# Kernel tuning notes

Hardware: AMD Instinct MI355X
Metric: run time of the kernel (lower is better)

The kernel has to match this reference:

```python
import jax, jax.numpy as jnp
import numpy as np

K = 1024          # codebook size
D = 64            # embedding dim
CC = 0.25         # commitment cost


def setup_inputs() -> dict:
    key = jax.random.key(0)
    k1, k2 = jax.random.split(key)
    inputs = jax.random.normal(k1, (64, 64, 32, 32), dtype=jnp.float32)  # [B, C=D, H, W]
    # nn.Embedding weight init: uniform(-1/K, 1/K)
    embedding = jax.random.uniform(k2, (K, D), dtype=jnp.float32,
                                   minval=-1.0 / K, maxval=1.0 / K)
    return {"inputs": inputs, "embedding": embedding}


def reference(inputs, embedding):
    # NCHW -> NHWC
    x = jnp.transpose(inputs, (0, 2, 3, 1))            # [B, H, W, D]
    B, H, W, Dd = x.shape
    flat = x.reshape(-1, Dd)                           # [N, D]
    distances = (jnp.sum(flat * flat, axis=1, keepdims=True)
                 - 2.0 * flat @ embedding.T
                 + jnp.sum(embedding * embedding, axis=1)[None, :])
    encoding_indices = jnp.argmin(distances, axis=1)   # [N]
    encodings = encoding_indices.reshape(B, H, W)      # [B, H, W]
    quantized = embedding[encodings]                   # [B, H, W, D]

    e_latent_loss = jnp.mean((jax.lax.stop_gradient(quantized) - x) ** 2)
    q_latent_loss = jnp.mean((quantized - jax.lax.stop_gradient(x)) ** 2)
    loss = q_latent_loss + CC * e_latent_loss

    # straight-through estimator
    quantized_st = x + jax.lax.stop_gradient(quantized - x)
    out = jnp.transpose(quantized_st, (0, 3, 1, 2))    # NHWC -> NCHW
    nll = jnp.ones((1,), dtype=jnp.float32)
    return out, encodings, loss, nll
```

## Files before the change

kernel.cpp:

```cpp
#include <hip/hip_runtime.h>
#include <stdint.h>

constexpr int KCODES = 1024;
constexpr int DDIM   = 64;
constexpr int HW     = 1024;
constexpr int NPTS   = 65536;
constexpr int PPB    = 64;
constexpr int NBLK   = NPTS / PPB;

constexpr int OUT_Q    = 0;
constexpr int OUT_IDX  = 4194304;
constexpr int OUT_LOSS = 4259840;
constexpr int OUT_NLL  = 4259841;

constexpr int WS_MAXC  = 0;
constexpr int WS_C     = 16;
constexpr int WS_E     = 2048;
constexpr int WS_PART  = 34816;

typedef __attribute__((ext_vector_type(8))) short short8v;
typedef __attribute__((ext_vector_type(4))) float float4v;

__device__ __forceinline__ uint16_t f2bf(float f) {
    uint32_t u = __float_as_uint(f);
    return (uint16_t)((u + 0x7fffu + ((u >> 16) & 1u)) >> 16);
}
__device__ __forceinline__ uint32_t pack2bf(float a, float b) {
    return (uint32_t)f2bf(a) | ((uint32_t)f2bf(b) << 16);
}

__device__ __forceinline__ float np_pairwise_sumsq64(const float* a) {
    float r[8];
    #pragma unroll
    for (int j = 0; j < 8; ++j) r[j] = __fmul_rn(a[j], a[j]);
    #pragma unroll
    for (int i = 8; i < 64; i += 8)
        #pragma unroll
        for (int j = 0; j < 8; ++j)
            r[j] = __fadd_rn(r[j], __fmul_rn(a[i + j], a[i + j]));
    return __fadd_rn(__fadd_rn(__fadd_rn(r[0], r[1]), __fadd_rn(r[2], r[3])),
                     __fadd_rn(__fadd_rn(r[4], r[5]), __fadd_rn(r[6], r[7])));
}

__global__ __launch_bounds__(256) void vq_init(const float* __restrict__ emb,
                                               float* __restrict__ ws) {
    __shared__ float smax[4];
    const int k = blockIdx.x * 256 + threadIdx.x;
    float row[DDIM];
    const float4* src = (const float4*)(emb + (size_t)k * DDIM);
    #pragma unroll
    for (int j = 0; j < 16; ++j) ((float4*)row)[j] = src[j];
    float C = np_pairwise_sumsq64(row);
    ws[WS_C + k] = C;
    {
        const int c = k >> 4, col = k & 15;
        uint32_t* eb = (uint32_t*)ws + WS_E + c * 512;
        #pragma unroll
        for (int q = 0; q < 4; ++q) {
            uint32_t* d0 = eb + (q * 16 + col) * 4;
            uint32_t* d1 = eb + 256 + (q * 16 + col) * 4;
            #pragma unroll
            for (int j = 0; j < 4; ++j) {
                d0[j] = pack2bf(row[q * 8 + 2 * j],      row[q * 8 + 2 * j + 1]);
                d1[j] = pack2bf(row[32 + q * 8 + 2 * j], row[32 + q * 8 + 2 * j + 1]);
            }
        }
    }
    float m = C;
    #pragma unroll
    for (int off = 32; off > 0; off >>= 1) m = fmaxf(m, __shfl_down(m, off, 64));
    if ((threadIdx.x & 63) == 0) smax[threadIdx.x >> 6] = m;
    __syncthreads();
    if (threadIdx.x == 0)
        ws[WS_MAXC + blockIdx.x] =
            fmaxf(fmaxf(smax[0], smax[1]), fmaxf(smax[2], smax[3]));
}

__global__ __launch_bounds__(256, 4) void vq_main(
        const float* __restrict__ inp, const float* __restrict__ emb,
        float* __restrict__ ws, float* __restrict__ out)
{
    __shared__ float    sAp[PPB][4];
    __shared__ float    sA[PPB];
    __shared__ float    sPart[4][PPB];
    __shared__ float    sThr[PPB];
    __shared__ uint16_t sCand[PPB * 4 * 8];
    __shared__ uint8_t  sCnt[PPB * 4];
    __shared__ int      sWin[PPB];
    __shared__ float    sred[4];

    const int tid  = threadIdx.x;
    const int lane = tid & 63;
    const int wave = tid >> 6;
    const int col  = lane & 15;
    const int quad = lane >> 4;
    const int base = blockIdx.x * PPB;
    const int b    = base >> 10;
    const int hw0  = base & 1023;

    {
        const int pp = tid >> 2;
        const int jj = (tid & 3) * 2;
        const float* xin = inp + (size_t)b * DDIM * HW + (hw0 + pp);
        float r0, r1;
        {
            float v0 = xin[(size_t)jj * HW];
            float v1 = xin[(size_t)(jj + 1) * HW];
            r0 = __fmul_rn(v0, v0);
            r1 = __fmul_rn(v1, v1);
        }
        #pragma unroll
        for (int i = 8; i < 64; i += 8) {
            float v0 = xin[(size_t)(i + jj) * HW];
            float v1 = xin[(size_t)(i + jj + 1) * HW];
            r0 = __fadd_rn(r0, __fmul_rn(v0, v0));
            r1 = __fadd_rn(r1, __fmul_rn(v1, v1));
        }
        sAp[pp][tid & 3] = __fadd_rn(r0, r1);
    }

    short8v a[4][2];
    #pragma unroll
    for (int g = 0; g < 4; ++g) {
        const float* xp = inp + (size_t)b * DDIM * HW + (hw0 + g * 16 + col);
        short8v t0, t1;
        #pragma unroll
        for (int j = 0; j < 8; ++j) {
            t0[j] = (short)f2bf(xp[(size_t)(quad * 8 + j) * HW]);
            t1[j] = (short)f2bf(xp[(size_t)(32 + quad * 8 + j) * HW]);
        }
        a[g][0] = t0; a[g][1] = t1;
    }

    const char* Eb = (const char*)((const uint32_t*)ws + WS_E);
    const char* Ew = Eb + (size_t)wave * 16 * 2048 + (size_t)lane * 16;
    const float* Cw = ws + WS_C;
    const int k0 = wave * 256;

    float smaxv[4][4];
    #pragma unroll
    for (int g = 0; g < 4; ++g)
        #pragma unroll
        for (int r = 0; r < 4; ++r) smaxv[g][r] = -3.0e38f;

    {
        short8v pa0 = *(const short8v*)(Ew);
        short8v pa1 = *(const short8v*)(Ew + 1024);
        short8v pb0 = *(const short8v*)(Ew + 2048);
        short8v pb1 = *(const short8v*)(Ew + 2048 + 1024);
        float   cia = Cw[k0 + col] * -0.5f;
        float   cib = Cw[k0 + 16 + col] * -0.5f;
        #pragma unroll 1
        for (int c2 = 0; c2 < 16; c2 += 2) {
            short8v u0 = pa0, u1 = pa1; float uci = cia;
            if (c2 + 2 < 16) {
                const char* er = Ew + (size_t)(c2 + 2) * 2048;
                pa0 = *(const short8v*)(er);
                pa1 = *(const short8v*)(er + 1024);
                cia = Cw[k0 + (c2 + 2) * 16 + col] * -0.5f;
            }
            float4v ci4 = {uci, uci, uci, uci};
            #pragma unroll
            for (int g = 0; g < 4; ++g) {
                float4v acc = ci4;
                acc = __builtin_amdgcn_mfma_f32_16x16x32_bf16(a[g][0], u0, acc, 0, 0, 0);
                acc = __builtin_amdgcn_mfma_f32_16x16x32_bf16(a[g][1], u1, acc, 0, 0, 0);
                #pragma unroll
                for (int r = 0; r < 4; ++r) smaxv[g][r] = fmaxf(smaxv[g][r], acc[r]);
            }
            short8v v0 = pb0, v1 = pb1; float vci = cib;
            if (c2 + 3 < 16) {
                const char* er = Ew + (size_t)(c2 + 3) * 2048;
                pb0 = *(const short8v*)(er);
                pb1 = *(const short8v*)(er + 1024);
                cib = Cw[k0 + (c2 + 3) * 16 + col] * -0.5f;
            }
            float4v ci4b = {vci, vci, vci, vci};
            #pragma unroll
            for (int g = 0; g < 4; ++g) {
                float4v acc = ci4b;
                acc = __builtin_amdgcn_mfma_f32_16x16x32_bf16(a[g][0], v0, acc, 0, 0, 0);
                acc = __builtin_amdgcn_mfma_f32_16x16x32_bf16(a[g][1], v1, acc, 0, 0, 0);
                #pragma unroll
                for (int r = 0; r < 4; ++r) smaxv[g][r] = fmaxf(smaxv[g][r], acc[r]);
            }
        }
    }
    #pragma unroll
    for (int g = 0; g < 4; ++g)
        #pragma unroll
        for (int r = 0; r < 4; ++r) {
            float m = smaxv[g][r];
            m = fmaxf(m, __shfl_xor(m, 1, 16));
            m = fmaxf(m, __shfl_xor(m, 2, 16));
            m = fmaxf(m, __shfl_xor(m, 4, 16));
            m = fmaxf(m, __shfl_xor(m, 8, 16));
            if (col == 0) sPart[wave][g * 16 + quad * 4 + r] = m;
        }
    __syncthreads();

    if (tid < PPB) {
        float A = __fadd_rn(__fadd_rn(sAp[tid][0], sAp[tid][1]),
                            __fadd_rn(sAp[tid][2], sAp[tid][3]));
        sA[tid] = A;
        float gm = fmaxf(fmaxf(sPart[0][tid], sPart[1][tid]),
                         fmaxf(sPart[2][tid], sPart[3][tid]));
        float mc = fmaxf(fmaxf(ws[WS_MAXC], ws[WS_MAXC + 1]),
                         fmaxf(ws[WS_MAXC + 2], ws[WS_MAXC + 3]));
        sThr[tid] = gm - (0.015625f * sqrtf(A) * sqrtf(mc) + 6e-5f);
    }
    __syncthreads();

    float thr[4][4];
    #pragma unroll
    for (int g = 0; g < 4; ++g)
        #pragma unroll
        for (int r = 0; r < 4; ++r) thr[g][r] = sThr[g * 16 + quad * 4 + r];

    int cnt[4][4];
    #pragma unroll
    for (int g = 0; g < 4; ++g)
        #pragma unroll
        for (int r = 0; r < 4; ++r) cnt[g][r] = 0;

    {
        short8v pa0 = *(const short8v*)(Ew);
        short8v pa1 = *(const short8v*)(Ew + 1024);
        short8v pb0 = *(const short8v*)(Ew + 2048);
        short8v pb1 = *(const short8v*)(Ew + 2048 + 1024);
        float   cia = Cw[k0 + col] * -0.5f;
        float   cib = Cw[k0 + 16 + col] * -0.5f;
        #pragma unroll 1
        for (int c2 = 0; c2 < 16; c2 += 2) {
            short8v u0 = pa0, u1 = pa1; float uci = cia;
            if (c2 + 2 < 16) {
                const char* er = Ew + (size_t)(c2 + 2) * 2048;
                pa0 = *(const short8v*)(er);
                pa1 = *(const short8v*)(er + 1024);
                cia = Cw[k0 + (c2 + 2) * 16 + col] * -0.5f;
            }
            float4v ci4 = {uci, uci, uci, uci};
            #pragma unroll
            for (int g = 0; g < 4; ++g) {
                float4v acc = ci4;
                acc = __builtin_amdgcn_mfma_f32_16x16x32_bf16(a[g][0], u0, acc, 0, 0, 0);
                acc = __builtin_amdgcn_mfma_f32_16x16x32_bf16(a[g][1], u1, acc, 0, 0, 0);
                #pragma unroll
                for (int r = 0; r < 4; ++r) {
                    unsigned long long bm = __ballot(acc[r] >= thr[g][r]);
                    if (col == 0) {
                        unsigned gm = (unsigned)(bm >> (quad * 16)) & 0xffffu;
                        while (gm) {
                            int bit = __ffs(gm) - 1;
                            gm &= gm - 1;
                            int ct = cnt[g][r];
                            if (ct < 8)
                                sCand[((g * 16 + quad * 4 + r) * 4 + wave) * 8 + ct] =
                                    (uint16_t)(k0 + c2 * 16 + bit);
                            cnt[g][r] = ct + 1;
                        }
                    }
                }
            }
            short8v v0 = pb0, v1 = pb1; float vci = cib;
            if (c2 + 3 < 16) {
                const char* er = Ew + (size_t)(c2 + 3) * 2048;
                pb0 = *(const short8v*)(er);
                pb1 = *(const short8v*)(er + 1024);
                cib = Cw[k0 + (c2 + 3) * 16 + col] * -0.5f;
            }
            float4v ci4b = {vci, vci, vci, vci};
            #pragma unroll
            for (int g = 0; g < 4; ++g) {
                float4v acc = ci4b;
                acc = __builtin_amdgcn_mfma_f32_16x16x32_bf16(a[g][0], v0, acc, 0, 0, 0);
                acc = __builtin_amdgcn_mfma_f32_16x16x32_bf16(a[g][1], v1, acc, 0, 0, 0);
                #pragma unroll
                for (int r = 0; r < 4; ++r) {
                    unsigned long long bm = __ballot(acc[r] >= thr[g][r]);
                    if (col == 0) {
                        unsigned gm = (unsigned)(bm >> (quad * 16)) & 0xffffu;
                        while (gm) {
                            int bit = __ffs(gm) - 1;
                            gm &= gm - 1;
                            int ct = cnt[g][r];
                            if (ct < 8)
                                sCand[((g * 16 + quad * 4 + r) * 4 + wave) * 8 + ct] =
                                    (uint16_t)(k0 + (c2 + 1) * 16 + bit);
                            cnt[g][r] = ct + 1;
                        }
                    }
                }
            }
        }
    }
    if (col == 0) {
        #pragma unroll
        for (int g = 0; g < 4; ++g)
            #pragma unroll
            for (int r = 0; r < 4; ++r) {
                int c = cnt[g][r];
                sCnt[(g * 16 + quad * 4 + r) * 4 + wave] = (uint8_t)(c > 255 ? 255 : c);
            }
    }
    __syncthreads();

    if (tid < PPB) {
        const int p = tid, n = base + p;
        int cq[4], tot = 0, cmax = 0;
        #pragma unroll
        for (int q = 0; q < 4; ++q) {
            cq[q] = sCnt[p * 4 + q];
            tot += cq[q];
            cmax = cq[q] > cmax ? cq[q] : cmax;
        }
        int win;
        if (tot == 1) {
            win = 0;
            #pragma unroll
            for (int q = 0; q < 4; ++q)
                if (cq[q]) win = sCand[(p * 4 + q) * 8];
        } else {
            const float* xin = inp + (size_t)b * DDIM * HW + (hw0 + p);
            float x[DDIM];
            #pragma unroll
            for (int d = 0; d < DDIM; ++d) x[d] = xin[(size_t)d * HW];
            const float A = sA[p];
            float bd = 3.0e38f; win = KCODES - 1;
            if (cmax <= 8) {
                #pragma unroll 1
                for (int q = 0; q < 4; ++q) {
                    #pragma unroll 1
                    for (int i = 0; i < cq[q]; ++i) {
                        int k = sCand[(p * 4 + q) * 8 + i];
                        float e[DDIM];
                        const float4* e4 = (const float4*)(emb + (size_t)k * DDIM);
                        #pragma unroll
                        for (int j = 0; j < 16; ++j) ((float4*)e)[j] = e4[j];
                        float g = 0.f;
                        #pragma unroll
                        for (int d = 0; d < DDIM; ++d) g = fmaf(x[d], e[d], g);
                        float dd = __fadd_rn(__fsub_rn(A, __fmul_rn(2.0f, g)), Cw[k]);
                        if (dd < bd || (dd == bd && k < win)) { bd = dd; win = k; }
                    }
                }
            } else {
                #pragma unroll 1
                for (int k = 0; k < KCODES; ++k) {
                    float e[DDIM];
                    const float4* e4 = (const float4*)(emb + (size_t)k * DDIM);
                    #pragma unroll
                    for (int j = 0; j < 16; ++j) ((float4*)e)[j] = e4[j];
                    float g = 0.f;
                    #pragma unroll
                    for (int d = 0; d < DDIM; ++d) g = fmaf(x[d], e[d], g);
                    float dd = __fadd_rn(__fsub_rn(A, __fmul_rn(2.0f, g)), Cw[k]);
                    if (dd < bd) { bd = dd; win = k; }
                }
            }
        }
        sWin[p] = win;
        out[OUT_IDX + n] = (float)win;
    }
    __syncthreads();

    {
        const int pl = tid & 63, qtr = tid >> 6;
        const int win = sWin[pl];
        const int ch0 = qtr * 16;
        float q[16];
        const float4* q4 = (const float4*)(emb + (size_t)win * DDIM + ch0);
        #pragma unroll
        for (int j = 0; j < 4; ++j) ((float4*)q)[j] = q4[j];
        const size_t off = (size_t)b * DDIM * HW + (size_t)ch0 * HW + (hw0 + pl);
        const float* xin2 = inp + off;
        float* orow = out + off;
        float lacc = 0.f;
        #pragma unroll
        for (int j = 0; j < 16; ++j) {
            float xv = xin2[(size_t)j * HW];
            float diff = __fsub_rn(q[j], xv);
            orow[(size_t)j * HW] = __fadd_rn(xv, diff);
            lacc = fmaf(diff, diff, lacc);
        }
        #pragma unroll
        for (int o2 = 32; o2 > 0; o2 >>= 1) lacc += __shfl_down(lacc, o2, 64);
        if (lane == 0) sred[wave] = lacc;
    }
    __syncthreads();
    if (tid == 0)
        ws[WS_PART + blockIdx.x] = sred[0] + sred[1] + sred[2] + sred[3];
}

__global__ __launch_bounds__(256) void vq_fin(const float* __restrict__ ws,
                                              float* __restrict__ out) {
    __shared__ float sred[4];
    const int tid = threadIdx.x;
    float s = 0.f;
    #pragma unroll
    for (int j = 0; j < 4; ++j) s += ws[WS_PART + j * 256 + tid];
    #pragma unroll
    for (int off = 32; off > 0; off >>= 1) s += __shfl_down(s, off, 64);
    if ((tid & 63) == 0) sred[tid >> 6] = s;
    __syncthreads();
    if (tid == 0) {
        float L = sred[0] + sred[1] + sred[2] + sred[3];
        out[OUT_LOSS] = L * (1.25f / 4194304.0f);
        out[OUT_NLL]  = 1.0f;
    }
}

extern "C" void kernel_launch(void* const* d_in, const int* in_sizes, int n_in,
                              void* d_out, int out_size, void* d_ws, size_t ws_size,
                              hipStream_t stream) {
    const float* inp = (const float*)d_in[0];
    const float* emb = (const float*)d_in[1];
    float* out = (float*)d_out;
    float* ws  = (float*)d_ws;

    vq_init<<<4, 256, 0, stream>>>(emb, ws);
    vq_main<<<NBLK, 256, 0, stream>>>(inp, emb, ws, out);
    vq_fin<<<1, 256, 0, stream>>>(ws, out);
}
```

Measured before the change: 119.8 us.

## Swap MFMA operands, per-lane candidate lists, and fold final loss reduction into main

Swaps the MFMA operand order so each lane's accumulator holds four codes for one point. The row max then becomes a local reduction plus two cross-quad shuffles, replacing the 16-lane shuffle tree. Candidate collection moves from per-row ballots with a serial col==0 loop to per-lane 64-bit packed lists of up to four indices, gated by a wave-wide any check. The separate final-reduction kernel is removed in favour of a last-block-done atomic counter, and the init kernel is reshaped to 16 blocks of 64 threads. The main risk is that the per-lane candidate cap drops from 8 to 4, which sends more points to the full 1024-code fallback scan.

```diff
diff --git a/kernel.cpp b/kernel.cpp
--- a/kernel.cpp
+++ b/kernel.cpp
@@ -17,6 +17,7 @@
 constexpr int WS_C     = 16;
 constexpr int WS_E     = 2048;
 constexpr int WS_PART  = 34816;
+constexpr int WS_CTR   = 35840;
 
 typedef __attribute__((ext_vector_type(8))) short short8v;
 typedef __attribute__((ext_vector_type(4))) float float4v;
@@ -42,10 +43,9 @@
                      __fadd_rn(__fadd_rn(r[4], r[5]), __fadd_rn(r[6], r[7])));
 }
 
-__global__ __launch_bounds__(256) void vq_init(const float* __restrict__ emb,
-                                               float* __restrict__ ws) {
-    __shared__ float smax[4];
-    const int k = blockIdx.x * 256 + threadIdx.x;
+__global__ __launch_bounds__(64) void vq_init(const float* __restrict__ emb,
+                                              float* __restrict__ ws) {
+    const int k = blockIdx.x * 64 + threadIdx.x;
     float row[DDIM];
     const float4* src = (const float4*)(emb + (size_t)k * DDIM);
     #pragma unroll
@@ -69,11 +69,8 @@
     float m = C;
     #pragma unroll
     for (int off = 32; off > 0; off >>= 1) m = fmaxf(m, __shfl_down(m, off, 64));
-    if ((threadIdx.x & 63) == 0) smax[threadIdx.x >> 6] = m;
-    __syncthreads();
-    if (threadIdx.x == 0)
-        ws[WS_MAXC + blockIdx.x] =
-            fmaxf(fmaxf(smax[0], smax[1]), fmaxf(smax[2], smax[3]));
+    if (threadIdx.x == 0) ws[WS_MAXC + blockIdx.x] = m;
+    if (k == 0) ((uint32_t*)ws)[WS_CTR] = 0u;
 }
 
 __global__ __launch_bounds__(256, 4) void vq_main(
@@ -84,10 +81,11 @@
     __shared__ float    sA[PPB];
     __shared__ float    sPart[4][PPB];
     __shared__ float    sThr[PPB];
-    __shared__ uint16_t sCand[PPB * 4 * 8];
-    __shared__ uint8_t  sCnt[PPB * 4];
+    __shared__ unsigned long long sCandL[16][PPB];
+    __shared__ int      sCntL[16][PPB];
     __shared__ int      sWin[PPB];
     __shared__ float    sred[4];
+    __shared__ int      sLast;
 
     const int tid  = threadIdx.x;
     const int lane = tid & 63;
@@ -136,67 +134,65 @@
     const char* Ew = Eb + (size_t)wave * 16 * 2048 + (size_t)lane * 16;
     const float* Cw = ws + WS_C;
     const int k0 = wave * 256;
-
-    float smaxv[4][4];
-    #pragma unroll
-    for (int g = 0; g < 4; ++g)
-        #pragma unroll
-        for (int r = 0; r < 4; ++r) smaxv[g][r] = -3.0e38f;
-
+    const float4v* Cq = (const float4v*)(ws + WS_C + k0);
+
+    float gmax[4] = {-3.0e38f, -3.0e38f, -3.0e38f, -3.0e38f};
     {
         short8v pa0 = *(const short8v*)(Ew);
         short8v pa1 = *(const short8v*)(Ew + 1024);
         short8v pb0 = *(const short8v*)(Ew + 2048);
-        short8v pb1 = *(const short8v*)(Ew + 2048 + 1024);
-        float   cia = Cw[k0 + col] * -0.5f;
-        float   cib = Cw[k0 + 16 + col] * -0.5f;
+        short8v pb1 = *(const short8v*)(Ew + 3072);
+        float4v ca4 = Cq[quad];
+        float4v cb4 = Cq[4 + quad];
         #pragma unroll 1
         for (int c2 = 0; c2 < 16; c2 += 2) {
-            short8v u0 = pa0, u1 = pa1; float uci = cia;
+            short8v u0 = pa0, u1 = pa1; float4v uc4 = ca4;
             if (c2 + 2 < 16) {
                 const char* er = Ew + (size_t)(c2 + 2) * 2048;
                 pa0 = *(const short8v*)(er);
                 pa1 = *(const short8v*)(er + 1024);
-                cia = Cw[k0 + (c2 + 2) * 16 + col] * -0.5f;
-            }
-            float4v ci4 = {uci, uci, uci, uci};
-            #pragma unroll
-            for (int g = 0; g < 4; ++g) {
-                float4v acc = ci4;
-                acc = __builtin_amdgcn_mfma_f32_16x16x32_bf16(a[g][0], u0, acc, 0, 0, 0);
-                acc = __builtin_amdgcn_mfma_f32_16x16x32_bf16(a[g][1], u1, acc, 0, 0, 0);
+                ca4 = Cq[(c2 + 2) * 4 + quad];
+            }
+            {
+                float4v ci = {uc4[0] * -0.5f, uc4[1] * -0.5f,
+                              uc4[2] * -0.5f, uc4[3] * -0.5f};
                 #pragma unroll
-                for (int r = 0; r < 4; ++r) smaxv[g][r] = fmaxf(smaxv[g][r], acc[r]);
-            }
-            short8v v0 = pb0, v1 = pb1; float vci = cib;
+                for (int g = 0; g < 4; ++g) {
+                    float4v acc = ci;
+                    acc = __builtin_amdgcn_mfma_f32_16x16x32_bf16(u0, a[g][0], acc, 0, 0, 0);
+                    acc = __builtin_amdgcn_mfma_f32_16x16x32_bf16(u1, a[g][1], acc, 0, 0, 0);
+                    gmax[g] = fmaxf(gmax[g],
+                                    fmaxf(fmaxf(acc[0], acc[1]), fmaxf(acc[2], acc[3])));
+                }
+            }
+            short8v v0 = pb0, v1 = pb1; float4v vc4 = cb4;
             if (c2 + 3 < 16) {
                 const char* er = Ew + (size_t)(c2 + 3) * 2048;
                 pb0 = *(const short8v*)(er);
                 pb1 = *(const short8v*)(er + 1024);
-                cib = Cw[k0 + (c2 + 3) * 16 + col] * -0.5f;
-            }
-            float4v ci4b = {vci, vci, vci, vci};
-            #pragma unroll
-            for (int g = 0; g < 4; ++g) {
-                float4v acc = ci4b;
-                acc = __builtin_amdgcn_mfma_f32_16x16x32_bf16(a[g][0], v0, acc, 0, 0, 0);
-                acc = __builtin_amdgcn_mfma_f32_16x16x32_bf16(a[g][1], v1, acc, 0, 0, 0);
+                cb4 = Cq[(c2 + 3) * 4 + quad];
+            }
+            {
+                float4v ci = {vc4[0] * -0.5f, vc4[1] * -0.5f,
+                              vc4[2] * -0.5f, vc4[3] * -0.5f};
                 #pragma unroll
-                for (int r = 0; r < 4; ++r) smaxv[g][r] = fmaxf(smaxv[g][r], acc[r]);
-            }
-        }
-    }
-    #pragma unroll
-    for (int g = 0; g < 4; ++g)
-        #pragma unroll
-        for (int r = 0; r < 4; ++r) {
-            float m = smaxv[g][r];
-            m = fmaxf(m, __shfl_xor(m, 1, 16));
-            m = fmaxf(m, __shfl_xor(m, 2, 16));
-            m = fmaxf(m, __shfl_xor(m, 4, 16));
-            m = fmaxf(m, __shfl_xor(m, 8, 16));
-            if (col == 0) sPart[wave][g * 16 + quad * 4 + r] = m;
-        }
+                for (int g = 0; g < 4; ++g) {
+                    float4v acc = ci;
+                    acc = __builtin_amdgcn_mfma_f32_16x16x32_bf16(v0, a[g][0], acc, 0, 0, 0);
+                    acc = __builtin_amdgcn_mfma_f32_16x16x32_bf16(v1, a[g][1], acc, 0, 0, 0);
+                    gmax[g] = fmaxf(gmax[g],
+                                    fmaxf(fmaxf(acc[0], acc[1]), fmaxf(acc[2], acc[3])));
+                }
+            }
+        }
+    }
+    #pragma unroll
+    for (int g = 0; g < 4; ++g) {
+        float m = gmax[g];
+        m = fmaxf(m, __shfl_xor(m, 16, 64));
+        m = fmaxf(m, __shfl_xor(m, 32, 64));
+        if (quad == 0) sPart[wave][g * 16 + col] = m;
+    }
     __syncthreads();
 
     if (tid < PPB) {
@@ -205,121 +201,115 @@
         sA[tid] = A;
         float gm = fmaxf(fmaxf(sPart[0][tid], sPart[1][tid]),
                          fmaxf(sPart[2][tid], sPart[3][tid]));
-        float mc = fmaxf(fmaxf(ws[WS_MAXC], ws[WS_MAXC + 1]),
-                         fmaxf(ws[WS_MAXC + 2], ws[WS_MAXC + 3]));
+        float mc = ws[WS_MAXC];
+        #pragma unroll
+        for (int j = 1; j < 16; ++j) mc = fmaxf(mc, ws[WS_MAXC + j]);
         sThr[tid] = gm - (0.015625f * sqrtf(A) * sqrtf(mc) + 6e-5f);
     }
     __syncthreads();
 
-    float thr[4][4];
-    #pragma unroll
-    for (int g = 0; g < 4; ++g)
-        #pragma unroll
-        for (int r = 0; r < 4; ++r) thr[g][r] = sThr[g * 16 + quad * 4 + r];
-
-    int cnt[4][4];
-    #pragma unroll
-    for (int g = 0; g < 4; ++g)
-        #pragma unroll
-        for (int r = 0; r < 4; ++r) cnt[g][r] = 0;
-
+    float thrg[4];
+    #pragma unroll
+    for (int g = 0; g < 4; ++g) thrg[g] = sThr[g * 16 + col];
+
+    unsigned long long lst[4] = {0ull, 0ull, 0ull, 0ull};
+    int cnt[4] = {0, 0, 0, 0};
     {
         short8v pa0 = *(const short8v*)(Ew);
         short8v pa1 = *(const short8v*)(Ew + 1024);
         short8v pb0 = *(const short8v*)(Ew + 2048);
-        short8v pb1 = *(const short8v*)(Ew + 2048 + 1024);
-        float   cia = Cw[k0 + col] * -0.5f;
-        float   cib = Cw[k0 + 16 + col] * -0.5f;
+        short8v pb1 = *(const short8v*)(Ew + 3072);
+        float4v ca4 = Cq[quad];
+        float4v cb4 = Cq[4 + quad];
         #pragma unroll 1
         for (int c2 = 0; c2 < 16; c2 += 2) {
-            short8v u0 = pa0, u1 = pa1; float uci = cia;
+            short8v u0 = pa0, u1 = pa1; float4v uc4 = ca4;
             if (c2 + 2 < 16) {
                 const char* er = Ew + (size_t)(c2 + 2) * 2048;
                 pa0 = *(const short8v*)(er);
                 pa1 = *(const short8v*)(er + 1024);
-                cia = Cw[k0 + (c2 + 2) * 16 + col] * -0.5f;
-            }
-            float4v ci4 = {uci, uci, uci, uci};
-            #pragma unroll
-            for (int g = 0; g < 4; ++g) {
-                float4v acc = ci4;
-                acc = __builtin_amdgcn_mfma_f32_16x16x32_bf16(a[g][0], u0, acc, 0, 0, 0);
-                acc = __builtin_amdgcn_mfma_f32_16x16x32_bf16(a[g][1], u1, acc, 0, 0, 0);
+                ca4 = Cq[(c2 + 2) * 4 + quad];
+            }
+            {
+                float4v ci = {uc4[0] * -0.5f, uc4[1] * -0.5f,
+                              uc4[2] * -0.5f, uc4[3] * -0.5f};
+                const int kb = k0 + c2 * 16 + quad * 4;
                 #pragma unroll
-                for (int r = 0; r < 4; ++r) {
-                    unsigned long long bm = __ballot(acc[r] >= thr[g][r]);
-                    if (col == 0) {
-                        unsigned gm = (unsigned)(bm >> (quad * 16)) & 0xffffu;
-                        while (gm) {
-                            int bit = __ffs(gm) - 1;
-                            gm &= gm - 1;
-                            int ct = cnt[g][r];
-                            if (ct < 8)
-                                sCand[((g * 16 + quad * 4 + r) * 4 + wave) * 8 + ct] =
-                                    (uint16_t)(k0 + c2 * 16 + bit);
-                            cnt[g][r] = ct + 1;
+                for (int g = 0; g < 4; ++g) {
+                    float4v acc = ci;
+                    acc = __builtin_amdgcn_mfma_f32_16x16x32_bf16(u0, a[g][0], acc, 0, 0, 0);
+                    acc = __builtin_amdgcn_mfma_f32_16x16x32_bf16(u1, a[g][1], acc, 0, 0, 0);
+                    float m4 = fmaxf(fmaxf(acc[0], acc[1]), fmaxf(acc[2], acc[3]));
+                    if (__any(m4 >= thrg[g])) {
+                        #pragma unroll
+                        for (int r = 0; r < 4; ++r) {
+                            if (acc[r] >= thrg[g]) {
+                                if (cnt[g] < 4)
+                                    lst[g] |= (unsigned long long)(unsigned)(kb + r)
+                                              << (cnt[g] << 4);
+                                ++cnt[g];
+                            }
                         }
                     }
                 }
             }
-            short8v v0 = pb0, v1 = pb1; float vci = cib;
+            short8v v0 = pb0, v1 = pb1; float4v vc4 = cb4;
             if (c2 + 3 < 16) {
                 const char* er = Ew + (size_t)(c2 + 3) * 2048;
                 pb0 = *(const short8v*)(er);
                 pb1 = *(const short8v*)(er + 1024);
-                cib = Cw[k0 + (c2 + 3) * 16 + col] * -0.5f;
-            }
-            float4v ci4b = {vci, vci, vci, vci};
-            #pragma unroll
-            for (int g = 0; g < 4; ++g) {
-                float4v acc = ci4b;
-                acc = __builtin_amdgcn_mfma_f32_16x16x32_bf16(a[g][0], v0, acc, 0, 0, 0);
-                acc = __builtin_amdgcn_mfma_f32_16x16x32_bf16(a[g][1], v1, acc, 0, 0, 0);
+                cb4 = Cq[(c2 + 3) * 4 + quad];
+            }
+            {
+                float4v ci = {vc4[0] * -0.5f, vc4[1] * -0.5f,
+                              vc4[2] * -0.5f, vc4[3] * -0.5f};
+                const int kb = k0 + (c2 + 1) * 16 + quad * 4;
                 #pragma unroll
-                for (int r = 0; r < 4; ++r) {
-                    unsigned long long bm = __ballot(acc[r] >= thr[g][r]);
-                    if (col == 0) {
-                        unsigned gm = (unsigned)(bm >> (quad * 16)) & 0xffffu;
-                        while (gm) {
-                            int bit = __ffs(gm) - 1;
-                            gm &= gm - 1;
-                            int ct = cnt[g][r];
-                            if (ct < 8)
-                                sCand[((g * 16 + quad * 4 + r) * 4 + wave) * 8 + ct] =
-                                    (uint16_t)(k0 + (c2 + 1) * 16 + bit);
-                            cnt[g][r] = ct + 1;
+                for (int g = 0; g < 4; ++g) {
+                    float4v acc = ci;
+                    acc = __builtin_amdgcn_mfma_f32_16x16x32_bf16(v0, a[g][0], acc, 0, 0, 0);
+                    acc = __builtin_amdgcn_mfma_f32_16x16x32_bf16(v1, a[g][1], acc, 0, 0, 0);
+                    float m4 = fmaxf(fmaxf(acc[0], acc[1]), fmaxf(acc[2], acc[3]));
+                    if (__any(m4 >= thrg[g])) {
+                        #pragma unroll
+                        for (int r = 0; r < 4; ++r) {
+                            if (acc[r] >= thrg[g]) {
+                                if (cnt[g] < 4)
+                                    lst[g] |= (unsigned long long)(unsigned)(kb + r)
+                                              << (cnt[g] << 4);
+                                ++cnt[g];
+                            }
                         }
                     }
                 }
             }
         }
     }
-    if (col == 0) {
-        #pragma unroll
-        for (int g = 0; g < 4; ++g)
-            #pragma unroll
-            for (int r = 0; r < 4; ++r) {
-                int c = cnt[g][r];
-                sCnt[(g * 16 + quad * 4 + r) * 4 + wave] = (uint8_t)(c > 255 ? 255 : c);
-            }
+    {
+        const int wq = wave * 4 + quad;
+        #pragma unroll
+        for (int g = 0; g < 4; ++g) {
+            sCandL[wq][g * 16 + col] = lst[g];
+            sCntL[wq][g * 16 + col]  = cnt[g];
+        }
     }
     __syncthreads();
 
     if (tid < PPB) {
         const int p = tid, n = base + p;
-        int cq[4], tot = 0, cmax = 0;
-        #pragma unroll
-        for (int q = 0; q < 4; ++q) {
-            cq[q] = sCnt[p * 4 + q];
-            tot += cq[q];
-            cmax = cq[q] > cmax ? cq[q] : cmax;
+        int tot = 0, cmax = 0;
+        #pragma unroll
+        for (int wq = 0; wq < 16; ++wq) {
+            int c = sCntL[wq][p];
+            tot += c;
+            cmax = c > cmax ? c : cmax;
         }
         int win;
         if (tot == 1) {
             win = 0;
             #pragma unroll
-            for (int q = 0; q < 4; ++q)
-                if (cq[q]) win = sCand[(p * 4 + q) * 8];
+            for (int wq = 0; wq < 16; ++wq)
+                if (sCntL[wq][p]) win = (int)(sCandL[wq][p] & 0xffffu);
         } else {
             const float* xin = inp + (size_t)b * DDIM * HW + (hw0 + p);
             float x[DDIM];
@@ -327,12 +317,15 @@
             for (int d = 0; d < DDIM; ++d) x[d] = xin[(size_t)d * HW];
             const float A = sA[p];
             float bd = 3.0e38f; win = KCODES - 1;
-            if (cmax <= 8) {
+            if (cmax <= 4) {
                 #pragma unroll 1
-                for (int q = 0; q < 4; ++q) {
+                for (int wq = 0; wq < 16; ++wq) {
+                    int c = sCntL[wq][p];
+                    unsigned long long L = sCandL[wq][p];
                     #pragma unroll 1
-                    for (int i = 0; i < cq[q]; ++i) {
-                        int k = sCand[(p * 4 + q) * 8 + i];
+                    for (int i = 0; i < c; ++i) {
+                        int k = (int)(L & 0xffffu);
+                        L >>= 16;
                         float e[DDIM];
                         const float4* e4 = (const float4*)(emb + (size_t)k * DDIM);
                         #pragma unroll
@@ -388,25 +381,28 @@
         if (lane == 0) sred[wave] = lacc;
     }
     __syncthreads();
-    if (tid == 0)
+
+    if (tid == 0) {
         ws[WS_PART + blockIdx.x] = sred[0] + sred[1] + sred[2] + sred[3];
-}
-
-__global__ __launch_bounds__(256) void vq_fin(const float* __restrict__ ws,
-                                              float* __restrict__ out) {
-    __shared__ float sred[4];
-    const int tid = threadIdx.x;
-    float s = 0.f;
-    #pragma unroll
-    for (int j = 0; j < 4; ++j) s += ws[WS_PART + j * 256 + tid];
-    #pragma unroll
-    for (int off = 32; off > 0; off >>= 1) s += __shfl_down(s, off, 64);
-    if ((tid & 63) == 0) sred[tid >> 6] = s;
-    __syncthreads();
-    if (tid == 0) {
-        float L = sred[0] + sred[1] + sred[2] + sred[3];
-        out[OUT_LOSS] = L * (1.25f / 4194304.0f);
-        out[OUT_NLL]  = 1.0f;
+        __threadfence();
+        unsigned int old = atomicAdd((unsigned int*)ws + WS_CTR, 1u);
+        sLast = (old == NBLK - 1) ? 1 : 0;
+    }
+    __syncthreads();
+    if (sLast) {
+        __threadfence();
+        float s = 0.f;
+        #pragma unroll
+        for (int j = 0; j < 4; ++j) s += ws[WS_PART + j * 256 + tid];
+        #pragma unroll
+        for (int off = 32; off > 0; off >>= 1) s += __shfl_down(s, off, 64);
+        if ((tid & 63) == 0) sred[tid >> 6] = s;
+        __syncthreads();
+        if (tid == 0) {
+            float L = sred[0] + sred[1] + sred[2] + sred[3];
+            out[OUT_LOSS] = L * (1.25f / 4194304.0f);
+            out[OUT_NLL]  = 1.0f;
+        }
     }
 }
 
@@ -418,7 +414,6 @@
     float* out = (float*)d_out;
     float* ws  = (float*)d_ws;
 
-    vq_init<<<4, 256, 0, stream>>>(emb, ws);
+    vq_init<<<16, 64, 0, stream>>>(emb, ws);
     vq_main<<<NBLK, 256, 0, stream>>>(inp, emb, ws, out);
-    vq_fin<<<1, 256, 0, stream>>>(ws, out);
-}
+}
```

Result: slower. 141.3 us (+17.9%).

## Split argmin and epilogue kernels, halve points per block, fold final reduction

Applied to the files above, without the earlier changes.

The main kernel is split in two. vq_argmin now processes 32 points per block, giving 2048 blocks for better occupancy and load spread. A separate vq_epi kernel writes the straight-through output and loss partials, and a last-block atomic counter replaces the separate final-reduction kernel. vq_init now uses 16 blocks of 64 threads. The cost is that the input tensor is re-read in the epilogue and the per-block codebook stream is amortized over fewer points, roughly doubling the bf16 codebook traffic from L2.

```diff
diff --git a/kernel.cpp b/kernel.cpp
--- a/kernel.cpp
+++ b/kernel.cpp
@@ -5,10 +5,11 @@
 constexpr int DDIM   = 64;
 constexpr int HW     = 1024;
 constexpr int NPTS   = 65536;
-constexpr int PPB    = 64;
-constexpr int NBLK   = NPTS / PPB;
-
-constexpr int OUT_Q    = 0;
+constexpr int PPB    = 32;
+constexpr int NBLK_A = NPTS / PPB;
+constexpr int EPB    = 64;
+constexpr int NBLK_E = NPTS / EPB;
+
 constexpr int OUT_IDX  = 4194304;
 constexpr int OUT_LOSS = 4259840;
 constexpr int OUT_NLL  = 4259841;
@@ -17,6 +18,7 @@
 constexpr int WS_C     = 16;
 constexpr int WS_E     = 2048;
 constexpr int WS_PART  = 34816;
+constexpr int WS_CTR   = 35840;
 
 typedef __attribute__((ext_vector_type(8))) short short8v;
 typedef __attribute__((ext_vector_type(4))) float float4v;
@@ -42,10 +44,9 @@
                      __fadd_rn(__fadd_rn(r[4], r[5]), __fadd_rn(r[6], r[7])));
 }
 
-__global__ __launch_bounds__(256) void vq_init(const float* __restrict__ emb,
-                                               float* __restrict__ ws) {
-    __shared__ float smax[4];
-    const int k = blockIdx.x * 256 + threadIdx.x;
+__global__ __launch_bounds__(64) void vq_init(const float* __restrict__ emb,
+                                              float* __restrict__ ws) {
+    const int k = blockIdx.x * 64 + threadIdx.x;
     float row[DDIM];
     const float4* src = (const float4*)(emb + (size_t)k * DDIM);
     #pragma unroll
@@ -69,25 +70,20 @@
     float m = C;
     #pragma unroll
     for (int off = 32; off > 0; off >>= 1) m = fmaxf(m, __shfl_down(m, off, 64));
-    if ((threadIdx.x & 63) == 0) smax[threadIdx.x >> 6] = m;
-    __syncthreads();
-    if (threadIdx.x == 0)
-        ws[WS_MAXC + blockIdx.x] =
-            fmaxf(fmaxf(smax[0], smax[1]), fmaxf(smax[2], smax[3]));
-}
-
-__global__ __launch_bounds__(256, 4) void vq_main(
+    if (threadIdx.x == 0) ws[WS_MAXC + blockIdx.x] = m;
+    if (k == 0) ((uint32_t*)ws)[WS_CTR] = 0u;
+}
+
+__global__ __launch_bounds__(256, 4) void vq_argmin(
         const float* __restrict__ inp, const float* __restrict__ emb,
         float* __restrict__ ws, float* __restrict__ out)
 {
-    __shared__ float    sAp[PPB][4];
+    __shared__ float    sAp[PPB][8];
     __shared__ float    sA[PPB];
     __shared__ float    sPart[4][PPB];
     __shared__ float    sThr[PPB];
     __shared__ uint16_t sCand[PPB * 4 * 8];
     __shared__ uint8_t  sCnt[PPB * 4];
-    __shared__ int      sWin[PPB];
-    __shared__ float    sred[4];
 
     const int tid  = threadIdx.x;
     const int lane = tid & 63;
@@ -99,29 +95,22 @@
     const int hw0  = base & 1023;
 
     {
-        const int pp = tid >> 2;
-        const int jj = (tid & 3) * 2;
+        const int pp  = tid & 31;
+        const int seg = tid >> 5;
         const float* xin = inp + (size_t)b * DDIM * HW + (hw0 + pp);
-        float r0, r1;
-        {
-            float v0 = xin[(size_t)jj * HW];
-            float v1 = xin[(size_t)(jj + 1) * HW];
-            r0 = __fmul_rn(v0, v0);
-            r1 = __fmul_rn(v1, v1);
-        }
-        #pragma unroll
-        for (int i = 8; i < 64; i += 8) {
-            float v0 = xin[(size_t)(i + jj) * HW];
-            float v1 = xin[(size_t)(i + jj + 1) * HW];
-            r0 = __fadd_rn(r0, __fmul_rn(v0, v0));
-            r1 = __fadd_rn(r1, __fmul_rn(v1, v1));
-        }
-        sAp[pp][tid & 3] = __fadd_rn(r0, r1);
-    }
-
-    short8v a[4][2];
-    #pragma unroll
-    for (int g = 0; g < 4; ++g) {
+        float v = xin[(size_t)seg * HW];
+        float r = __fmul_rn(v, v);
+        #pragma unroll
+        for (int i = 1; i < 8; ++i) {
+            float vv = xin[(size_t)(8 * i + seg) * HW];
+            r = __fadd_rn(r, __fmul_rn(vv, vv));
+        }
+        sAp[pp][seg] = r;
+    }
+
+    short8v a[2][2];
+    #pragma unroll
+    for (int g = 0; g < 2; ++g) {
         const float* xp = inp + (size_t)b * DDIM * HW + (hw0 + g * 16 + col);
         short8v t0, t1;
         #pragma unroll
@@ -137,9 +126,9 @@
     const float* Cw = ws + WS_C;
     const int k0 = wave * 256;
 
-    float smaxv[4][4];
-    #pragma unroll
-    for (int g = 0; g < 4; ++g)
+    float smaxv[2][4];
+    #pragma unroll
+    for (int g = 0; g < 2; ++g)
         #pragma unroll
         for (int r = 0; r < 4; ++r) smaxv[g][r] = -3.0e38f;
 
@@ -147,7 +136,7 @@
         short8v pa0 = *(const short8v*)(Ew);
         short8v pa1 = *(const short8v*)(Ew + 1024);
         short8v pb0 = *(const short8v*)(Ew + 2048);
-        short8v pb1 = *(const short8v*)(Ew + 2048 + 1024);
+        short8v pb1 = *(const short8v*)(Ew + 3072);
         float   cia = Cw[k0 + col] * -0.5f;
         float   cib = Cw[k0 + 16 + col] * -0.5f;
         #pragma unroll 1
@@ -161,7 +150,7 @@
             }
             float4v ci4 = {uci, uci, uci, uci};
             #pragma unroll
-            for (int g = 0; g < 4; ++g) {
+            for (int g = 0; g < 2; ++g) {
                 float4v acc = ci4;
                 acc = __builtin_amdgcn_mfma_f32_16x16x32_bf16(a[g][0], u0, acc, 0, 0, 0);
                 acc = __builtin_amdgcn_mfma_f32_16x16x32_bf16(a[g][1], u1, acc, 0, 0, 0);
@@ -177,7 +166,7 @@
             }
             float4v ci4b = {vci, vci, vci, vci};
             #pragma unroll
-            for (int g = 0; g < 4; ++g) {
+            for (int g = 0; g < 2; ++g) {
                 float4v acc = ci4b;
                 acc = __builtin_amdgcn_mfma_f32_16x16x32_bf16(a[g][0], v0, acc, 0, 0, 0);
                 acc = __builtin_amdgcn_mfma_f32_16x16x32_bf16(a[g][1], v1, acc, 0, 0, 0);
@@ -187,7 +176,7 @@
         }
     }
     #pragma unroll
-    for (int g = 0; g < 4; ++g)
+    for (int g = 0; g < 2; ++g)
         #pragma unroll
         for (int r = 0; r < 4; ++r) {
             float m = smaxv[g][r];
@@ -200,26 +189,30 @@
     __syncthreads();
 
     if (tid < PPB) {
-        float A = __fadd_rn(__fadd_rn(sAp[tid][0], sAp[tid][1]),
-                            __fadd_rn(sAp[tid][2], sAp[tid][3]));
+        float A = __fadd_rn(
+            __fadd_rn(__fadd_rn(sAp[tid][0], sAp[tid][1]),
+                      __fadd_rn(sAp[tid][2], sAp[tid][3])),
+            __fadd_rn(__fadd_rn(sAp[tid][4], sAp[tid][5]),
+                      __fadd_rn(sAp[tid][6], sAp[tid][7])));
         sA[tid] = A;
         float gm = fmaxf(fmaxf(sPart[0][tid], sPart[1][tid]),
                          fmaxf(sPart[2][tid], sPart[3][tid]));
-        float mc = fmaxf(fmaxf(ws[WS_MAXC], ws[WS_MAXC + 1]),
-                         fmaxf(ws[WS_MAXC + 2], ws[WS_MAXC + 3]));
+        float mc = ws[WS_MAXC];
+        #pragma unroll
+        for (int j = 1; j < 16; ++j) mc = fmaxf(mc, ws[WS_MAXC + j]);
         sThr[tid] = gm - (0.015625f * sqrtf(A) * sqrtf(mc) + 6e-5f);
     }
     __syncthreads();
 
-    float thr[4][4];
-    #pragma unroll
-    for (int g = 0; g < 4; ++g)
+    float thr[2][4];
+    #pragma unroll
+    for (int g = 0; g < 2; ++g)
         #pragma unroll
         for (int r = 0; r < 4; ++r) thr[g][r] = sThr[g * 16 + quad * 4 + r];
 
-    int cnt[4][4];
-    #pragma unroll
-    for (int g = 0; g < 4; ++g)
+    int cnt[2][4];
+    #pragma unroll
+    for (int g = 0; g < 2; ++g)
         #pragma unroll
         for (int r = 0; r < 4; ++r) cnt[g][r] = 0;
 
@@ -227,7 +220,7 @@
         short8v pa0 = *(const short8v*)(Ew);
         short8v pa1 = *(const short8v*)(Ew + 1024);
         short8v pb0 = *(const short8v*)(Ew + 2048);
-        short8v pb1 = *(const short8v*)(Ew + 2048 + 1024);
+        short8v pb1 = *(const short8v*)(Ew + 3072);
         float   cia = Cw[k0 + col] * -0.5f;
         float   cib = Cw[k0 + 16 + col] * -0.5f;
         #pragma unroll 1
@@ -241,7 +234,7 @@
             }
             float4v ci4 = {uci, uci, uci, uci};
             #pragma unroll
-            for (int g = 0; g < 4; ++g) {
+            for (int g = 0; g < 2; ++g) {
                 float4v acc = ci4;
                 acc = __builtin_amdgcn_mfma_f32_16x16x32_bf16(a[g][0], u0, acc, 0, 0, 0);
                 acc = __builtin_amdgcn_mfma_f32_16x16x32_bf16(a[g][1], u1, acc, 0, 0, 0);
@@ -271,7 +264,7 @@
             }
             float4v ci4b = {vci, vci, vci, vci};
             #pragma unroll
-            for (int g = 0; g < 4; ++g) {
+            for (int g = 0; g < 2; ++g) {
                 float4v acc = ci4b;
                 acc = __builtin_amdgcn_mfma_f32_16x16x32_bf16(a[g][0], v0, acc, 0, 0, 0);
                 acc = __builtin_amdgcn_mfma_f32_16x16x32_bf16(a[g][1], v1, acc, 0, 0, 0);
@@ -296,7 +289,7 @@
     }
     if (col == 0) {
         #pragma unroll
-        for (int g = 0; g < 4; ++g)
+        for (int g = 0; g < 2; ++g)
             #pragma unroll
             for (int r = 0; r < 4; ++r) {
                 int c = cnt[g][r];
@@ -359,14 +352,27 @@
                 }
             }
         }
-        sWin[p] = win;
         out[OUT_IDX + n] = (float)win;
     }
-    __syncthreads();
+}
+
+__global__ __launch_bounds__(256, 4) void vq_epi(
+        const float* __restrict__ inp, const float* __restrict__ emb,
+        float* __restrict__ ws, float* __restrict__ out)
+{
+    __shared__ float sred[4];
+    __shared__ int   sLast;
+
+    const int tid  = threadIdx.x;
+    const int lane = tid & 63;
+    const int wave = tid >> 6;
+    const int base = blockIdx.x * EPB;
+    const int b    = base >> 10;
+    const int hw0  = base & 1023;
 
     {
         const int pl = tid & 63, qtr = tid >> 6;
-        const int win = sWin[pl];
+        const int win = (int)out[OUT_IDX + base + pl];
         const int ch0 = qtr * 16;
         float q[16];
         const float4* q4 = (const float4*)(emb + (size_t)win * DDIM + ch0);
@@ -388,25 +394,28 @@
         if (lane == 0) sred[wave] = lacc;
     }
     __syncthreads();
-    if (tid == 0)
+
+    if (tid == 0) {
         ws[WS_PART + blockIdx.x] = sred[0] + sred[1] + sred[2] + sred[3];
-}
-
-__global__ __launch_bounds__(256) void vq_fin(const float* __restrict__ ws,
-                                              float* __restrict__ out) {
-    __shared__ float sred[4];
-    const int tid = threadIdx.x;
-    float s = 0.f;
-    #pragma unroll
-    for (int j = 0; j < 4; ++j) s += ws[WS_PART + j * 256 + tid];
-    #pragma unroll
-    for (int off = 32; off > 0; off >>= 1) s += __shfl_down(s, off, 64);
-    if ((tid & 63) == 0) sred[tid >> 6] = s;
+        __threadfence();
+        unsigned int old = atomicAdd((unsigned int*)ws + WS_CTR, 1u);
+        sLast = (old == NBLK_E - 1) ? 1 : 0;
+    }
     __syncthreads();
-    if (tid == 0) {
-        float L = sred[0] + sred[1] + sred[2] + sred[3];
-        out[OUT_LOSS] = L * (1.25f / 4194304.0f);
-        out[OUT_NLL]  = 1.0f;
+    if (sLast) {
+        __threadfence();
+        float s = 0.f;
+        #pragma unroll
+        for (int j = 0; j < 4; ++j) s += ws[WS_PART + j * 256 + tid];
+        #pragma unroll
+        for (int off = 32; off > 0; off >>= 1) s += __shfl_down(s, off, 64);
+        if ((tid & 63) == 0) sred[tid >> 6] = s;
+        __syncthreads();
+        if (tid == 0) {
+            float L = sred[0] + sred[1] + sred[2] + sred[3];
+            out[OUT_LOSS] = L * (1.25f / 4194304.0f);
+            out[OUT_NLL]  = 1.0f;
+        }
     }
 }
 
@@ -418,7 +427,7 @@
     float* out = (float*)d_out;
     float* ws  = (float*)d_ws;
 
-    vq_init<<<4, 256, 0, stream>>>(emb, ws);
-    vq_main<<<NBLK, 256, 0, stream>>>(inp, emb, ws, out);
-    vq_fin<<<1, 256, 0, stream>>>(ws, out);
-}
+    vq_init<<<16, 64, 0, stream>>>(emb, ws);
+    vq_argmin<<<NBLK_A, 256, 0, stream>>>(inp, emb, ws, out);
+    vq_epi<<<NBLK_E, 256, 0, stream>>>(inp, emb, ws, out);
+}
```

After: 165.1 us. 37.8% more time.
